# Optimization experiments

Measured on AMD Instinct MI355X. Metric: run time of the kernel, lower is better.

The kernel has to match this reference:

```python
import jax, jax.numpy as jnp
import numpy as np

NUM_SAMPLES = 512
FG_FRAC = 0.25
BATCH = 64
N = 131072


def _subsample(key, indicator, labels):
    """Faithful port of BalancedPositiveNegativeSampler._static_subsample.

    indicator: bool [N] sample candidates; labels: bool [N] positive flags.
    Returns int32 [N] indicator of sampled examples (1 = sampled).
    """
    n = indicator.shape[0]
    # Pad indicator with extra False examples so at least NUM_SAMPLES are True.
    num_true = jnp.sum(indicator.astype(jnp.float32))
    additional_false = jnp.cumsum((~indicator).astype(jnp.float32)) <= (NUM_SAMPLES - num_true)
    ind = indicator | additional_false
    # Random shuffle (permutation stored to restore order post-sampling).
    perm = jax.random.permutation(key, n)
    ind_p = ind[perm]
    lab_p = labels[perm]
    # 1-based index where indicator True, 0 otherwise; sign by label.
    idx = jnp.where(ind_p, jnp.arange(1, n + 1, dtype=jnp.int32), jnp.int32(0))
    signed = jnp.where(lab_p, jnp.int32(1), jnp.int32(-1))
    s_idx = idx * signed
    # Descending sort: positives first, then zeros, then negatives (most-negative last).
    sorted_desc = jnp.flip(jnp.sort(s_idx))
    # Balanced pos/neg counts.
    num_pos_avail = jnp.sum((sorted_desc > 0).astype(jnp.int32))
    max_pos = jnp.int32(int(NUM_SAMPLES * FG_FRAC))
    num_pos = jnp.minimum(max_pos, num_pos_avail)
    # Take first num_pos from the start and (NUM_SAMPLES - num_pos) from the end.
    rk = jnp.arange(NUM_SAMPLES, dtype=jnp.int32)
    gather_idx = jnp.where(rk < num_pos, rk, n - NUM_SAMPLES + rk)
    sampled = sorted_desc[gather_idx]
    # Back to 0-based indices; clamp empty slots to 0.
    sampled = jnp.abs(sampled) - 1
    sampled = jnp.where(sampled >= 0, sampled, 0)
    # Indicator in shuffled order, then scatter back through the permutation.
    ind2 = jnp.zeros(n, jnp.int32).at[sampled].set(1)
    out = jnp.zeros(n, jnp.int32).at[perm].set(ind2)
    return out


def setup_inputs() -> dict:
    key = jax.random.key(0)
    k1, k2, k3 = jax.random.split(key, 3)
    positive_matches = jax.random.bernoulli(k1, 0.01, (BATCH, N))
    negative_matches = jax.random.bernoulli(k2, 0.70, (BATCH, N)) & (~positive_matches)
    ignored_matches = jax.random.bernoulli(k3, 0.05, (BATCH, N)) & (~positive_matches) & (~negative_matches)
    return {
        "positive_matches": positive_matches,
        "negative_matches": negative_matches,
        "ignored_matches": ignored_matches,
    }


def reference(positive_matches, negative_matches, ignored_matches):
    b = positive_matches.shape[0]
    candidates = (positive_matches | negative_matches) & (~ignored_matches)
    keys = jax.random.split(jax.random.key(42), b)
    sampled_indicators = jax.vmap(_subsample)(keys, candidates, positive_matches)  # int32 [B, N]
    # Final top_k over {0,1} indicators: selected indices first (ascending), then rest.
    _, selected_indices = jax.lax.top_k(sampled_indicators, NUM_SAMPLES)
    return selected_indices
```

## Files before the change

kernel.cpp:

```cpp
#include <hip/hip_runtime.h>
#include <stdint.h>

#define BATCH 64
#define NN 131072
#define NCOARSE 256
#define SLOT 1024
#define CHUNK 4096
#define NSUB 1024
#define EMASK17 0x1FFFFu
#define CAP 1024
#define CCAP 256

typedef uint32_t u32;
typedef uint64_t u64;

__device__ __forceinline__ u32 rotl32(u32 v, int d) { return (v << d) | (v >> (32 - d)); }

__device__ __forceinline__ void threefry2x32(u32 k0, u32 k1, u32 x0, u32 x1, u32& o0, u32& o1) {
  u32 ks2 = k0 ^ k1 ^ 0x1BD11BDAu;
  x0 += k0; x1 += k1;
#define TF_R(r) { x0 += x1; x1 = rotl32(x1, r); x1 ^= x0; }
  TF_R(13) TF_R(15) TF_R(26) TF_R(6)
  x0 += k1;  x1 += ks2 + 1u;
  TF_R(17) TF_R(29) TF_R(16) TF_R(24)
  x0 += ks2; x1 += k0 + 2u;
  TF_R(13) TF_R(15) TF_R(26) TF_R(6)
  x0 += k0;  x1 += k1 + 3u;
  TF_R(17) TF_R(29) TF_R(16) TF_R(24)
  x0 += k1;  x1 += ks2 + 4u;
  TF_R(13) TF_R(15) TF_R(26) TF_R(6)
  x0 += ks2; x1 += k0 + 5u;
#undef TF_R
  o0 = x0; o1 = x1;
}

__device__ __forceinline__ u32 tf_bits(u32 k0, u32 k1, u32 i) {
  u32 o0, o1;
  threefry2x32(k0, k1, 0u, i, o0, o1);
  return o0 ^ o1;
}

__device__ void batch_round_key(int b, int round, u32& rk0, u32& rk1) {
  u32 kb0, kb1;
  threefry2x32(0u, 42u, 0u, (u32)b, kb0, kb1);
  if (round == 1) { threefry2x32(kb0, kb1, 0u, 1u, rk0, rk1); return; }
  u32 c0, c1;
  threefry2x32(kb0, kb1, 0u, 0u, c0, c1);
  threefry2x32(c0, c1, 0u, 1u, rk0, rk1);
}

__global__ __launch_bounds__(256) void scatterA_kernel(u32* __restrict__ cursor, u64* __restrict__ binned,
                                                       const int* __restrict__ posg, const int* __restrict__ negg,
                                                       const int* __restrict__ igng, int batch0) {
  __shared__ u32 sk[2];
  __shared__ u32 hist[NCOARSE];
  __shared__ u32 lstart[NCOARSE];
  __shared__ u32 gbase[NCOARSE];
  __shared__ u64 staged[CHUNK];
  __shared__ u32 stmp[NCOARSE];
  int g = blockIdx.y;
  int b = batch0 + g;
  int tid = threadIdx.x;
  if (tid == 0) { u32 k0, k1; batch_round_key(b, 1, k0, k1); sk[0] = k0; sk[1] = k1; }
  if (tid < NCOARSE) hist[tid] = 0;
  __syncthreads();
  u32 base = blockIdx.x * CHUNK;
  u64 recs[16]; u32 rr[16];
  const int4* P4 = (const int4*)(posg + (size_t)b * NN);
  const int4* Q4 = (const int4*)(negg + (size_t)b * NN);
  const int4* I4 = (const int4*)(igng + (size_t)b * NN);
#pragma unroll
  for (int j = 0; j < 4; j++) {
    u32 e0 = base + j * 1024 + tid * 4;
    int4 pv = P4[e0 >> 2];
    int4 nv = Q4[e0 >> 2];
    int4 iv = I4[e0 >> 2];
#pragma unroll
    for (int m = 0; m < 4; m++) {
      u32 e = e0 + m;
      int p = (&pv.x)[m] != 0, n = (&nv.x)[m] != 0, ig = (&iv.x)[m] != 0;
      u32 label = ((p | n) && !ig) ? (p ? 1u : 2u) : 0u;
      u32 k1 = tf_bits(sk[0], sk[1], e);
      u32 bin = k1 >> 24;
      rr[j * 4 + m] = atomicAdd(&hist[bin], 1u);
      recs[j * 4 + m] = ((u64)k1 << 19) | ((u64)e << 2) | (u64)label;
    }
  }
  __syncthreads();
  if (tid < NCOARSE) stmp[tid] = hist[tid];
  __syncthreads();
  for (int off = 1; off < NCOARSE; off <<= 1) {
    u32 t = 0;
    if (tid < NCOARSE && tid >= off) t = stmp[tid - off];
    __syncthreads();
    if (tid < NCOARSE) stmp[tid] += t;
    __syncthreads();
  }
  if (tid < NCOARSE) lstart[tid] = stmp[tid] - hist[tid];
  __syncthreads();
#pragma unroll
  for (int j = 0; j < 16; j++) {
    u32 bin = (u32)(recs[j] >> 43);
    staged[lstart[bin] + rr[j]] = recs[j];
  }
  if (tid < NCOARSE) {
    u32 c = hist[tid];
    gbase[tid] = c ? atomicAdd(&cursor[(size_t)g * NCOARSE + tid], c) : 0u;
  }
  __syncthreads();
  u64* bn = binned + (size_t)g * NCOARSE * SLOT;
  for (int s = tid; s < CHUNK; s += 256) {
    u64 v = staged[s];
    u32 bin = (u32)(v >> 43);
    u32 dst = bin * SLOT + gbase[bin] + ((u32)s - lstart[bin]);
    bn[dst] = v;
  }
}

__global__ __launch_bounds__(256) void scanB_kernel(const u32* __restrict__ cursor, u32* __restrict__ starts) {
  __shared__ u32 stmp[NCOARSE];
  __shared__ u32 cnts[NCOARSE];
  int g = blockIdx.x, tid = threadIdx.x;
  u32 v = cursor[(size_t)g * NCOARSE + tid];
  cnts[tid] = v; stmp[tid] = v;
  __syncthreads();
  for (int off = 1; off < NCOARSE; off <<= 1) {
    u32 t = (tid >= off) ? stmp[tid - off] : 0u;
    __syncthreads();
    stmp[tid] += t;
    __syncthreads();
  }
  starts[(size_t)g * NCOARSE + tid] = stmp[tid] - cnts[tid];
}

__global__ __launch_bounds__(512) void passB_kernel(const u32* __restrict__ cursor, const u32* __restrict__ starts,
                                                    const u64* __restrict__ binned, u64* __restrict__ EL,
                                                    u32* __restrict__ posh, u32* __restrict__ negh, int batch0) {
  __shared__ u32 sk2[2];
  __shared__ u64 keys[SLOT];
  __shared__ u32 hist[NSUB];
  __shared__ u32 sstart[NSUB];
  __shared__ u32 wtot[8];
  __shared__ u32 lpos[NCOARSE], lneg[NCOARSE];
  int g = blockIdx.y;
  int tid = threadIdx.x;
  if (tid == 0) {
    u32 a, c;
    batch_round_key(batch0 + g, 2, a, c); sk2[0] = a; sk2[1] = c;
  }
  if (tid < NCOARSE) { lpos[tid] = 0; lneg[tid] = 0; }
  __syncthreads();
  const u64* bn = binned + (size_t)g * NCOARSE * SLOT;
  u64* el = EL + (size_t)g * NN;
  for (int q = 0; q < 8; q++) {
    u32 bin = blockIdx.x * 8 + q;
    u32 cnt = cursor[(size_t)g * NCOARSE + bin];
    if (cnt > SLOT) cnt = SLOT;
    u32 start = starts[(size_t)g * NCOARSE + bin];
    hist[tid] = 0; hist[tid + 512] = 0;
    __syncthreads();
    u64 mykey[2]; u32 mysr[2];
#pragma unroll
    for (int t = 0; t < 2; t++) {
      int i = tid + t * 512;
      if (i < (int)cnt) {
        u64 key = bn[bin * SLOT + i];
        u32 sub = (u32)(key >> 33) & 0x3FFu;
        u32 r = atomicAdd(&hist[sub], 1u);
        mykey[t] = key;
        mysr[t] = (sub << 10) | r;
      } else {
        mysr[t] = 0xFFFFFFFFu;
      }
    }
    __syncthreads();
    u32 h0 = hist[2 * tid], h1 = hist[2 * tid + 1];
    u32 s = h0 + h1;
    u32 v = s;
#pragma unroll
    for (int off = 1; off < 64; off <<= 1) {
      u32 t2 = __shfl_up(v, off, 64);
      if ((tid & 63) >= off) v += t2;
    }
    if ((tid & 63) == 63) wtot[tid >> 6] = v;
    __syncthreads();
    u32 woff = 0;
    for (int w = 0; w < (tid >> 6); w++) woff += wtot[w];
    u32 excl = v + woff - s;
    sstart[2 * tid] = excl;
    sstart[2 * tid + 1] = excl + h0;
    __syncthreads();
#pragma unroll
    for (int t = 0; t < 2; t++) {
      if (mysr[t] != 0xFFFFFFFFu)
        keys[sstart[mysr[t] >> 10] + (mysr[t] & 0x3FFu)] = mykey[t];
    }
    __syncthreads();
#pragma unroll
    for (int t = 0; t < 2; t++) {
      int i = tid + t * 512;
      if (i < (int)cnt) {
        u64 ki = keys[i];
        u32 sub = (u32)(ki >> 33) & 0x3FFu;
        u32 s0 = sstart[sub], h = hist[sub];
        u32 r = 0;
        for (u32 j = s0; j < s0 + h; j++) {
          if (keys[j] < ki) r++;
        }
        u32 p1 = start + s0 + r;
        u32 e = (u32)(ki >> 2) & EMASK17;
        u32 label = (u32)ki & 3u;
        u32 k2 = 0;
        if (label) {
          k2 = tf_bits(sk2[0], sk2[1], p1);
          if (label == 1) atomicAdd(&lpos[k2 >> 24], 1u);
          else atomicAdd(&lneg[k2 >> 24], 1u);
        }
        el[p1] = ((u64)k2 << 32) | ((u64)e << 2) | (u64)label;
      }
    }
    __syncthreads();
  }
  if (tid < NCOARSE) {
    if (lpos[tid]) atomicAdd(&posh[(size_t)g * NCOARSE + tid], lpos[tid]);
  } else if (tid < 2 * NCOARSE) {
    int t = tid - NCOARSE;
    if (lneg[t]) atomicAdd(&negh[(size_t)g * NCOARSE + t], lneg[t]);
  }
}

__global__ __launch_bounds__(256) void threshold_kernel(const u32* __restrict__ posh,
                                                        const u32* __restrict__ negh,
                                                        u32* __restrict__ params) {
  int g = blockIdx.x, tid = threadIdx.x;
  __shared__ u32 rp[NCOARSE], rn[NCOARSE];
  rp[tid] = posh[(size_t)g * NCOARSE + tid];
  rn[tid] = negh[(size_t)g * NCOARSE + tid];
  __syncthreads();
  if (tid == 0) {
    u32 np = 0;
    for (int i = 0; i < NCOARSE; i++) np += rp[i];
    u32 qp = np < 128 ? np : 128;
    u32 qn = 512 - qp;
    u32 tp = 256;
    if (qp > 0) {
      u32 cum = 0;
      for (int i = 255; i >= 0; i--) { cum += rp[i]; if (cum >= qp) { tp = (u32)i; break; } }
    }
    u32 tn = 0, cum = 0;
    for (int i = 255; i >= 0; i--) { cum += rn[i]; if (cum >= qn) { tn = (u32)i; break; } }
    u32* pr = params + (size_t)g * 4;
    pr[0] = tp; pr[1] = tn; pr[2] = qp; pr[3] = qn;
  }
}

__global__ __launch_bounds__(256) void collect_kernel(const u64* __restrict__ EL, const u32* __restrict__ params,
                                                      u32* __restrict__ cnt, u64* __restrict__ poskey,
                                                      u32* __restrict__ posval, u64* __restrict__ negkey,
                                                      u32* __restrict__ negval, int batch0) {
  __shared__ u32 sp[2];
  __shared__ u32 lcnt[2];
  __shared__ u32 lbase[2];
  __shared__ u64 skey[2][CCAP];
  __shared__ u32 sval[2][CCAP];
  int g = blockIdx.y;
  int tid = threadIdx.x;
  if (tid == 0) {
    const u32* pr = params + (size_t)g * 4; sp[0] = pr[0]; sp[1] = pr[1];
    lcnt[0] = 0; lcnt[1] = 0;
  }
  __syncthreads();
  const u64* el = EL + (size_t)g * NN;
#pragma unroll
  for (int c = 0; c < 16; c++) {
    u32 p1 = blockIdx.x * CHUNK + c * 256 + tid;
    u64 v = el[p1];
    u32 label = (u32)v & 3u;
    if (!label) continue;
    u32 k2 = (u32)(v >> 32);
    int li = (int)label - 1;
    if ((k2 >> 24) >= sp[li]) {
      u32 val = ((u32)(v >> 2) & EMASK17) | (label << 17);
      u32 r = atomicAdd(&lcnt[li], 1u);
      if (r < CCAP) {
        skey[li][r] = (v & 0xFFFFFFFF00000000ull) | p1;
        sval[li][r] = val;
      } else {
        u32 s = atomicAdd(&cnt[(size_t)g * 16 + li], 1u);
        if (s < CAP) {
          if (li == 0) { poskey[(size_t)g * CAP + s] = ((u64)k2 << 32) | p1; posval[(size_t)g * CAP + s] = val; }
          else { negkey[(size_t)g * CAP + s] = ((u64)k2 << 32) | p1; negval[(size_t)g * CAP + s] = val; }
        }
      }
    }
  }
  __syncthreads();
  if (tid < 2) {
    u32 n = lcnt[tid]; if (n > CCAP) n = CCAP;
    lbase[tid] = n ? atomicAdd(&cnt[(size_t)g * 16 + tid], n) : 0u;
  }
  __syncthreads();
#pragma unroll
  for (int li = 0; li < 2; li++) {
    u32 n = lcnt[li]; if (n > CCAP) n = CCAP;
    u64* gk = li ? negkey : poskey;
    u32* gv = li ? negval : posval;
    for (u32 i = tid; i < n; i += 256) {
      u32 s = lbase[li] + i;
      if (s < CAP) { gk[(size_t)g * CAP + s] = skey[li][i]; gv[(size_t)g * CAP + s] = sval[li][i]; }
    }
  }
}

__global__ __launch_bounds__(1024) void select_final_kernel(const u32* __restrict__ params,
                                                            const u32* __restrict__ cnt,
                                                            const u64* __restrict__ poskey,
                                                            const u32* __restrict__ posval,
                                                            const u64* __restrict__ negkey,
                                                            const u32* __restrict__ negval,
                                                            int* __restrict__ out, int batch0) {
  int g = blockIdx.x, tid = threadIdx.x, b = batch0 + g;
  __shared__ u64 skey[1024];
  __shared__ u32 sval[1024];
  __shared__ int sel[512];
  const u32* pr = params + (size_t)g * 4;
  u32 qp = pr[2], qn = pr[3];
  u32 cp = cnt[(size_t)g * 16]; if (cp > CAP) cp = CAP;
  u32 cn = cnt[(size_t)g * 16 + 1]; if (cn > CAP) cn = CAP;
  if (tid < 512) sel[tid] = 0;

  skey[tid] = (tid < (int)cp) ? poskey[(size_t)g * CAP + tid] : 0ull;
  sval[tid] = (tid < (int)cp) ? posval[(size_t)g * CAP + tid] : 0u;
  __syncthreads();
  for (int k = 2; k <= 1024; k <<= 1)
    for (int s = k >> 1; s > 0; s >>= 1) {
      if (tid < 512) {
        int i = ((tid & ~(s - 1)) << 1) | (tid & (s - 1));
        int j = i | s;
        bool up = ((i & k) == 0);
        if ((skey[i] < skey[j]) == up) {
          u64 tk = skey[i]; skey[i] = skey[j]; skey[j] = tk;
          u32 tv = sval[i]; sval[i] = sval[j]; sval[j] = tv;
        }
      }
      __syncthreads();
    }
  if (tid < (int)qp) sel[tid] = (int)(sval[tid] & EMASK17);
  __syncthreads();

  skey[tid] = (tid < (int)cn) ? negkey[(size_t)g * CAP + tid] : 0ull;
  sval[tid] = (tid < (int)cn) ? negval[(size_t)g * CAP + tid] : 0u;
  __syncthreads();
  for (int k = 2; k <= 1024; k <<= 1)
    for (int s = k >> 1; s > 0; s >>= 1) {
      if (tid < 512) {
        int i = ((tid & ~(s - 1)) << 1) | (tid & (s - 1));
        int j = i | s;
        bool up = ((i & k) == 0);
        if ((skey[i] < skey[j]) == up) {
          u64 tk = skey[i]; skey[i] = skey[j]; skey[j] = tk;
          u32 tv = sval[i]; sval[i] = sval[j]; sval[j] = tv;
        }
      }
      __syncthreads();
    }
  if (tid < (int)qn) sel[qp + tid] = (int)(sval[tid] & EMASK17);
  __syncthreads();

  for (int k = 2; k <= 512; k <<= 1)
    for (int s = k >> 1; s > 0; s >>= 1) {
      if (tid < 256) {
        int i = ((tid & ~(s - 1)) << 1) | (tid & (s - 1));
        int j = i | s;
        bool up = ((i & k) == 0);
        int a = sel[i], c = sel[j];
        if ((a > c) == up) { sel[i] = c; sel[j] = a; }
      }
      __syncthreads();
    }
  if (tid < 512) out[(size_t)b * 512 + tid] = sel[tid];
}

extern "C" void kernel_launch(void* const* d_in, const int* in_sizes, int n_in,
                              void* d_out, int out_size, void* d_ws, size_t ws_size,
                              hipStream_t stream) {
  const int* pos = (const int*)d_in[0];
  const int* neg = (const int*)d_in[1];
  const int* ign = (const int*)d_in[2];
  int* out = (int*)d_out;

  size_t zeroPer = (NCOARSE * 3 + 16) * 4;
  size_t perBatch = zeroPer + (size_t)NCOARSE * SLOT * 8 + (size_t)NN * 8 + NCOARSE * 4 + 16 +
                    (size_t)CAP * (8 + 8 + 4 + 4);
  int G = (int)(ws_size / perBatch);
  if (G > BATCH) G = BATCH;
  if (G < 1) G = 1;

  char* p = (char*)d_ws;
  u32* cursor = (u32*)p;            p += (size_t)G * NCOARSE * 4;
  u32* posh = (u32*)p;              p += (size_t)G * NCOARSE * 4;
  u32* negh = (u32*)p;              p += (size_t)G * NCOARSE * 4;
  u32* cnt = (u32*)p;               p += (size_t)G * 16 * 4;
  size_t zeroBytes = (size_t)p - (size_t)d_ws;
  u64* binned = (u64*)p;            p += (size_t)G * NCOARSE * SLOT * 8;
  u64* EL = (u64*)p;                p += (size_t)G * NN * 8;
  u32* starts = (u32*)p;            p += (size_t)G * NCOARSE * 4;
  u32* params = (u32*)p;            p += (size_t)G * 4 * 4;
  u64* poskey = (u64*)p;            p += (size_t)G * CAP * 8;
  u64* negkey = (u64*)p;            p += (size_t)G * CAP * 8;
  u32* posval = (u32*)p;            p += (size_t)G * CAP * 4;
  u32* negval = (u32*)p;            p += (size_t)G * CAP * 4;

  for (int batch0 = 0; batch0 < BATCH; batch0 += G) {
    int Gi = (BATCH - batch0 < G) ? (BATCH - batch0) : G;
    hipMemsetAsync(d_ws, 0, zeroBytes, stream);
    dim3 gridS(NN / CHUNK, Gi);
    scatterA_kernel<<<gridS, 256, 0, stream>>>(cursor, binned, pos, neg, ign, batch0);
    scanB_kernel<<<Gi, 256, 0, stream>>>(cursor, starts);
    dim3 gridP(NCOARSE / 8, Gi);
    passB_kernel<<<gridP, 512, 0, stream>>>(cursor, starts, binned, EL, posh, negh, batch0);
    threshold_kernel<<<Gi, 256, 0, stream>>>(posh, negh, params);
    dim3 gridC(NN / CHUNK, Gi);
    collect_kernel<<<gridC, 256, 0, stream>>>(EL, params, cnt, poskey, posval, negkey, negval, batch0);
    select_final_kernel<<<Gi, 1024, 0, stream>>>(params, cnt, poskey, posval, negkey, negval, out, batch0);
  }
}
```

Before: 256.9 us.

## Compress binned and EL records to 32-bit keys, recompute hashes on tie

```diff
diff --git a/kernel.cpp b/kernel.cpp
--- a/kernel.cpp
+++ b/kernel.cpp
@@ -4,7 +4,7 @@
 #define BATCH 64
 #define NN 131072
 #define NCOARSE 256
-#define SLOT 1024
+#define SLOT 768
 #define CHUNK 4096
 #define NSUB 1024
 #define EMASK17 0x1FFFFu
@@ -49,7 +49,7 @@
   threefry2x32(c0, c1, 0u, 1u, rk0, rk1);
 }
 
-__global__ __launch_bounds__(256) void scatterA_kernel(u32* __restrict__ cursor, u64* __restrict__ binned,
+__global__ __launch_bounds__(256) void scatterA_kernel(u32* __restrict__ cursor, u32* __restrict__ binned,
                                                        const int* __restrict__ posg, const int* __restrict__ negg,
                                                        const int* __restrict__ igng, int batch0) {
   __shared__ u32 sk[2];
@@ -108,12 +108,14 @@
     gbase[tid] = c ? atomicAdd(&cursor[(size_t)g * NCOARSE + tid], c) : 0u;
   }
   __syncthreads();
-  u64* bn = binned + (size_t)g * NCOARSE * SLOT;
+  u32* bn = binned + (size_t)g * NCOARSE * SLOT;
   for (int s = tid; s < CHUNK; s += 256) {
     u64 v = staged[s];
-    u32 bin = (u32)(v >> 43);
-    u32 dst = bin * SLOT + gbase[bin] + ((u32)s - lstart[bin]);
-    bn[dst] = v;
+    u32 k1 = (u32)(v >> 19);
+    u32 bin = k1 >> 24;
+    u32 off = gbase[bin] + ((u32)s - lstart[bin]);
+    if (off < SLOT)
+      bn[bin * SLOT + off] = (((k1 >> 11) & 0x1FFFu) << 19) | ((u32)v & 0x7FFFFu);
   }
 }
 
@@ -134,10 +136,10 @@
 }
 
 __global__ __launch_bounds__(512) void passB_kernel(const u32* __restrict__ cursor, const u32* __restrict__ starts,
-                                                    const u64* __restrict__ binned, u64* __restrict__ EL,
+                                                    const u32* __restrict__ binned, u32* __restrict__ EL,
                                                     u32* __restrict__ posh, u32* __restrict__ negh, int batch0) {
-  __shared__ u32 sk2[2];
-  __shared__ u64 keys[SLOT];
+  __shared__ u32 sk1[2], sk2[2];
+  __shared__ u32 keys[SLOT];
   __shared__ u32 hist[NSUB];
   __shared__ u32 sstart[NSUB];
   __shared__ u32 wtot[8];
@@ -146,12 +148,13 @@
   int tid = threadIdx.x;
   if (tid == 0) {
     u32 a, c;
+    batch_round_key(batch0 + g, 1, a, c); sk1[0] = a; sk1[1] = c;
     batch_round_key(batch0 + g, 2, a, c); sk2[0] = a; sk2[1] = c;
   }
   if (tid < NCOARSE) { lpos[tid] = 0; lneg[tid] = 0; }
   __syncthreads();
-  const u64* bn = binned + (size_t)g * NCOARSE * SLOT;
-  u64* el = EL + (size_t)g * NN;
+  const u32* bn = binned + (size_t)g * NCOARSE * SLOT;
+  u32* el = EL + (size_t)g * NN;
   for (int q = 0; q < 8; q++) {
     u32 bin = blockIdx.x * 8 + q;
     u32 cnt = cursor[(size_t)g * NCOARSE + bin];
@@ -159,13 +162,13 @@
     u32 start = starts[(size_t)g * NCOARSE + bin];
     hist[tid] = 0; hist[tid + 512] = 0;
     __syncthreads();
-    u64 mykey[2]; u32 mysr[2];
+    u32 mykey[2]; u32 mysr[2];
 #pragma unroll
     for (int t = 0; t < 2; t++) {
       int i = tid + t * 512;
       if (i < (int)cnt) {
-        u64 key = bn[bin * SLOT + i];
-        u32 sub = (u32)(key >> 33) & 0x3FFu;
+        u32 key = bn[bin * SLOT + i];
+        u32 sub = key >> 22;
         u32 r = atomicAdd(&hist[sub], 1u);
         mykey[t] = key;
         mysr[t] = (sub << 10) | r;
@@ -196,29 +199,51 @@
         keys[sstart[mysr[t] >> 10] + (mysr[t] & 0x3FFu)] = mykey[t];
     }
     __syncthreads();
+    u32 lp1[2], pay[2];
 #pragma unroll
     for (int t = 0; t < 2; t++) {
       int i = tid + t * 512;
+      lp1[t] = 0xFFFFFFFFu;
       if (i < (int)cnt) {
-        u64 ki = keys[i];
-        u32 sub = (u32)(ki >> 33) & 0x3FFu;
+        u32 ki = keys[i];
+        u32 sub = ki >> 22;
         u32 s0 = sstart[sub], h = hist[sub];
+        u32 ei = (ki >> 2) & EMASK17;
         u32 r = 0;
         for (u32 j = s0; j < s0 + h; j++) {
-          if (keys[j] < ki) r++;
+          if ((int)j == i) continue;
+          u32 kj = keys[j];
+          bool lt;
+          if ((kj ^ ki) >> 19) {
+            lt = kj < ki;
+          } else {
+            u32 ej = (kj >> 2) & EMASK17;
+            u32 k1j = tf_bits(sk1[0], sk1[1], ej);
+            u32 k1i = tf_bits(sk1[0], sk1[1], ei);
+            lt = (k1j < k1i) || (k1j == k1i && ej < ei);
+          }
+          if (lt) r++;
         }
-        u32 p1 = start + s0 + r;
-        u32 e = (u32)(ki >> 2) & EMASK17;
-        u32 label = (u32)ki & 3u;
+        u32 local = s0 + r;
+        u32 p1 = start + local;
+        u32 label = ki & 3u;
         u32 k2 = 0;
         if (label) {
           k2 = tf_bits(sk2[0], sk2[1], p1);
           if (label == 1) atomicAdd(&lpos[k2 >> 24], 1u);
           else atomicAdd(&lneg[k2 >> 24], 1u);
         }
-        el[p1] = ((u64)k2 << 32) | ((u64)e << 2) | (u64)label;
-      }
-    }
+        lp1[t] = local;
+        pay[t] = (k2 & 0xFFF80000u) | (ei << 2) | label;
+      }
+    }
+    __syncthreads();
+#pragma unroll
+    for (int t = 0; t < 2; t++) {
+      if (lp1[t] != 0xFFFFFFFFu) keys[lp1[t]] = pay[t];
+    }
+    __syncthreads();
+    for (u32 i = tid; i < cnt; i += 512) el[start + i] = keys[i];
     __syncthreads();
   }
   if (tid < NCOARSE) {
@@ -254,15 +279,15 @@
   }
 }
 
-__global__ __launch_bounds__(256) void collect_kernel(const u64* __restrict__ EL, const u32* __restrict__ params,
-                                                      u32* __restrict__ cnt, u64* __restrict__ poskey,
-                                                      u32* __restrict__ posval, u64* __restrict__ negkey,
-                                                      u32* __restrict__ negval, int batch0) {
+__global__ __launch_bounds__(256) void collect_kernel(const u32* __restrict__ EL, const u32* __restrict__ params,
+                                                      u32* __restrict__ cnt, u32* __restrict__ posp1,
+                                                      u32* __restrict__ pose, u32* __restrict__ negp1,
+                                                      u32* __restrict__ nege, int batch0) {
   __shared__ u32 sp[2];
   __shared__ u32 lcnt[2];
   __shared__ u32 lbase[2];
-  __shared__ u64 skey[2][CCAP];
-  __shared__ u32 sval[2][CCAP];
+  __shared__ u32 lp1b[2][CCAP];
+  __shared__ u32 leb[2][CCAP];
   int g = blockIdx.y;
   int tid = threadIdx.x;
   if (tid == 0) {
@@ -270,26 +295,29 @@
     lcnt[0] = 0; lcnt[1] = 0;
   }
   __syncthreads();
-  const u64* el = EL + (size_t)g * NN;
-#pragma unroll
-  for (int c = 0; c < 16; c++) {
-    u32 p1 = blockIdx.x * CHUNK + c * 256 + tid;
-    u64 v = el[p1];
-    u32 label = (u32)v & 3u;
-    if (!label) continue;
-    u32 k2 = (u32)(v >> 32);
-    int li = (int)label - 1;
-    if ((k2 >> 24) >= sp[li]) {
-      u32 val = ((u32)(v >> 2) & EMASK17) | (label << 17);
-      u32 r = atomicAdd(&lcnt[li], 1u);
-      if (r < CCAP) {
-        skey[li][r] = (v & 0xFFFFFFFF00000000ull) | p1;
-        sval[li][r] = val;
-      } else {
-        u32 s = atomicAdd(&cnt[(size_t)g * 16 + li], 1u);
-        if (s < CAP) {
-          if (li == 0) { poskey[(size_t)g * CAP + s] = ((u64)k2 << 32) | p1; posval[(size_t)g * CAP + s] = val; }
-          else { negkey[(size_t)g * CAP + s] = ((u64)k2 << 32) | p1; negval[(size_t)g * CAP + s] = val; }
+  const uint4* el4 = (const uint4*)(EL + (size_t)g * NN);
+#pragma unroll
+  for (int c = 0; c < 4; c++) {
+    u32 i4 = blockIdx.x * 1024 + c * 256 + tid;
+    uint4 v4 = el4[i4];
+#pragma unroll
+    for (int m = 0; m < 4; m++) {
+      u32 val = (&v4.x)[m];
+      u32 label = val & 3u;
+      if (!label) continue;
+      int li = (int)label - 1;
+      if ((val >> 24) >= sp[li]) {
+        u32 p1 = i4 * 4 + m;
+        u32 e = (val >> 2) & EMASK17;
+        u32 r = atomicAdd(&lcnt[li], 1u);
+        if (r < CCAP) {
+          lp1b[li][r] = p1; leb[li][r] = e;
+        } else {
+          u32 s = atomicAdd(&cnt[(size_t)g * 16 + li], 1u);
+          if (s < CAP) {
+            if (li == 0) { posp1[(size_t)g * CAP + s] = p1; pose[(size_t)g * CAP + s] = e; }
+            else { negp1[(size_t)g * CAP + s] = p1; nege[(size_t)g * CAP + s] = e; }
+          }
         }
       }
     }
@@ -303,34 +331,40 @@
 #pragma unroll
   for (int li = 0; li < 2; li++) {
     u32 n = lcnt[li]; if (n > CCAP) n = CCAP;
-    u64* gk = li ? negkey : poskey;
-    u32* gv = li ? negval : posval;
+    u32* gp = li ? negp1 : posp1;
+    u32* ge = li ? nege : pose;
     for (u32 i = tid; i < n; i += 256) {
       u32 s = lbase[li] + i;
-      if (s < CAP) { gk[(size_t)g * CAP + s] = skey[li][i]; gv[(size_t)g * CAP + s] = sval[li][i]; }
+      if (s < CAP) { gp[(size_t)g * CAP + s] = lp1b[li][i]; ge[(size_t)g * CAP + s] = leb[li][i]; }
     }
   }
 }
 
 __global__ __launch_bounds__(1024) void select_final_kernel(const u32* __restrict__ params,
                                                             const u32* __restrict__ cnt,
-                                                            const u64* __restrict__ poskey,
-                                                            const u32* __restrict__ posval,
-                                                            const u64* __restrict__ negkey,
-                                                            const u32* __restrict__ negval,
+                                                            const u32* __restrict__ posp1,
+                                                            const u32* __restrict__ pose,
+                                                            const u32* __restrict__ negp1,
+                                                            const u32* __restrict__ nege,
                                                             int* __restrict__ out, int batch0) {
   int g = blockIdx.x, tid = threadIdx.x, b = batch0 + g;
+  __shared__ u32 sk2[2];
   __shared__ u64 skey[1024];
   __shared__ u32 sval[1024];
   __shared__ int sel[512];
+  if (tid == 0) { u32 a, c; batch_round_key(b, 2, a, c); sk2[0] = a; sk2[1] = c; }
   const u32* pr = params + (size_t)g * 4;
   u32 qp = pr[2], qn = pr[3];
   u32 cp = cnt[(size_t)g * 16]; if (cp > CAP) cp = CAP;
   u32 cn = cnt[(size_t)g * 16 + 1]; if (cn > CAP) cn = CAP;
   if (tid < 512) sel[tid] = 0;
-
-  skey[tid] = (tid < (int)cp) ? poskey[(size_t)g * CAP + tid] : 0ull;
-  sval[tid] = (tid < (int)cp) ? posval[(size_t)g * CAP + tid] : 0u;
+  __syncthreads();
+
+  if (tid < (int)cp) {
+    u32 p1 = posp1[(size_t)g * CAP + tid];
+    skey[tid] = ((u64)tf_bits(sk2[0], sk2[1], p1) << 32) | p1;
+    sval[tid] = pose[(size_t)g * CAP + tid];
+  } else { skey[tid] = 0ull; sval[tid] = 0u; }
   __syncthreads();
   for (int k = 2; k <= 1024; k <<= 1)
     for (int s = k >> 1; s > 0; s >>= 1) {
@@ -345,11 +379,14 @@
       }
       __syncthreads();
     }
-  if (tid < (int)qp) sel[tid] = (int)(sval[tid] & EMASK17);
-  __syncthreads();
-
-  skey[tid] = (tid < (int)cn) ? negkey[(size_t)g * CAP + tid] : 0ull;
-  sval[tid] = (tid < (int)cn) ? negval[(size_t)g * CAP + tid] : 0u;
+  if (tid < (int)qp) sel[tid] = (int)sval[tid];
+  __syncthreads();
+
+  if (tid < (int)cn) {
+    u32 p1 = negp1[(size_t)g * CAP + tid];
+    skey[tid] = ((u64)tf_bits(sk2[0], sk2[1], p1) << 32) | p1;
+    sval[tid] = nege[(size_t)g * CAP + tid];
+  } else { skey[tid] = 0ull; sval[tid] = 0u; }
   __syncthreads();
   for (int k = 2; k <= 1024; k <<= 1)
     for (int s = k >> 1; s > 0; s >>= 1) {
@@ -364,7 +401,7 @@
       }
       __syncthreads();
     }
-  if (tid < (int)qn) sel[qp + tid] = (int)(sval[tid] & EMASK17);
+  if (tid < (int)qn) sel[qp + tid] = (int)sval[tid];
   __syncthreads();
 
   for (int k = 2; k <= 512; k <<= 1)
@@ -390,8 +427,8 @@
   int* out = (int*)d_out;
 
   size_t zeroPer = (NCOARSE * 3 + 16) * 4;
-  size_t perBatch = zeroPer + (size_t)NCOARSE * SLOT * 8 + (size_t)NN * 8 + NCOARSE * 4 + 16 +
-                    (size_t)CAP * (8 + 8 + 4 + 4);
+  size_t perBatch = zeroPer + (size_t)NCOARSE * SLOT * 4 + (size_t)NN * 4 + NCOARSE * 4 + 16 +
+                    (size_t)CAP * 4 * 4;
   int G = (int)(ws_size / perBatch);
   if (G > BATCH) G = BATCH;
   if (G < 1) G = 1;
@@ -402,14 +439,14 @@
   u32* negh = (u32*)p;              p += (size_t)G * NCOARSE * 4;
   u32* cnt = (u32*)p;               p += (size_t)G * 16 * 4;
   size_t zeroBytes = (size_t)p - (size_t)d_ws;
-  u64* binned = (u64*)p;            p += (size_t)G * NCOARSE * SLOT * 8;
-  u64* EL = (u64*)p;                p += (size_t)G * NN * 8;
+  u32* binned = (u32*)p;            p += (size_t)G * NCOARSE * SLOT * 4;
+  u32* EL = (u32*)p;                p += (size_t)G * NN * 4;
   u32* starts = (u32*)p;            p += (size_t)G * NCOARSE * 4;
   u32* params = (u32*)p;            p += (size_t)G * 4 * 4;
-  u64* poskey = (u64*)p;            p += (size_t)G * CAP * 8;
-  u64* negkey = (u64*)p;            p += (size_t)G * CAP * 8;
-  u32* posval = (u32*)p;            p += (size_t)G * CAP * 4;
-  u32* negval = (u32*)p;            p += (size_t)G * CAP * 4;
+  u32* posp1 = (u32*)p;             p += (size_t)G * CAP * 4;
+  u32* pose = (u32*)p;              p += (size_t)G * CAP * 4;
+  u32* negp1 = (u32*)p;             p += (size_t)G * CAP * 4;
+  u32* nege = (u32*)p;              p += (size_t)G * CAP * 4;
 
   for (int batch0 = 0; batch0 < BATCH; batch0 += G) {
     int Gi = (BATCH - batch0 < G) ? (BATCH - batch0) : G;
@@ -421,7 +458,7 @@
     passB_kernel<<<gridP, 512, 0, stream>>>(cursor, starts, binned, EL, posh, negh, batch0);
     threshold_kernel<<<Gi, 256, 0, stream>>>(posh, negh, params);
     dim3 gridC(NN / CHUNK, Gi);
-    collect_kernel<<<gridC, 256, 0, stream>>>(EL, params, cnt, poskey, posval, negkey, negval, batch0);
-    select_final_kernel<<<Gi, 1024, 0, stream>>>(params, cnt, poskey, posval, negkey, negval, out, batch0);
-  }
-}
+    collect_kernel<<<gridC, 256, 0, stream>>>(EL, params, cnt, posp1, pose, negp1, nege, batch0);
+    select_final_kernel<<<Gi, 1024, 0, stream>>>(params, cnt, posp1, pose, negp1, nege, out, batch0);
+  }
+}
```

Measured after the change: 310.6 us. +20.9%, slower.
